# Performance work log

Hardware: AMD Instinct MI355X
Metric: run time of the kernel (lower is better)

## Reference

```python
import jax, jax.numpy as jnp
import numpy as np

WS = 8   # window_size
SS = 4   # shift_size
NH = 8   # num_heads


def _shift_mask(ws, ss):
    """Faithful port of _create_shift_mask (returns [1,1,ws,ws])."""
    m = np.zeros((ws, ws), np.float32)
    cnt = 0
    for hs in (slice(0, ws - ss), slice(ws - ss, ws)):
        for wsl in (slice(0, ws - ss), slice(ws - ss, ws)):
            m[hs, wsl] = cnt
            cnt += 1
    shifted = np.roll(m, (-ss, -ss), (0, 1))
    return (m != shifted).astype(np.float32)[None, None]

_MASK = jnp.asarray(_shift_mask(WS, SS))  # all-ones when ss == ws/2 (as in source)


def window_partition(x, ws):
    # [B,C,H,W] -> [B*nWin, C, ws, ws]
    B, C, H, W = x.shape
    x = x.reshape(B, C, H // ws, ws, W // ws, ws)
    x = x.transpose(0, 2, 4, 1, 3, 5)
    return x.reshape(-1, C, ws, ws)


def window_merge(x, H, W, ws):
    # [B*nWin, C, ws, ws] -> [B,C,H,W]
    C = x.shape[1]
    B = x.shape[0] // ((H // ws) * (W // ws))
    x = x.reshape(B, H // ws, W // ws, C, ws, ws)
    x = x.transpose(0, 3, 1, 4, 2, 5)
    return x.reshape(B, C, H, W)


def conv1x1(x, w):
    # 1x1 conv, no bias: weight [Cout, Cin]
    return jnp.einsum('oc,bchw->bohw', w, x)


def win_attention(q, k, v, temperature):
    # q,k,v: [Bw, C, ws, ws]; temperature: [nh,1,1]
    Bw, C, wh, ww = q.shape
    hd = C // NH
    N = wh * ww
    def heads(t):
        return t.reshape(Bw, NH, hd, N).transpose(0, 1, 3, 2)  # [Bw,nh,N,hd]
    q, k, v = heads(q), heads(k), heads(v)
    attn = jnp.einsum('bhnd,bhmd->bhnm', q, k) * temperature  # temp broadcasts per-head
    attn = jax.nn.softmax(attn, axis=-1)
    out = jnp.einsum('bhnm,bhmd->bhnd', attn, v)
    return out.transpose(0, 1, 3, 2).reshape(Bw, C, wh, ww)


def _branch(x_q, x_kv, temperature, Wq, Wk, Wv, Wo):
    xq_w = window_partition(x_q, WS)
    xkv_w = window_partition(x_kv, WS)
    q = conv1x1(xq_w, Wq)
    k = conv1x1(xkv_w, Wk)
    v = conv1x1(xkv_w, Wv)
    a = win_attention(q, k, v, temperature)
    return conv1x1(a, Wo)  # [B*nWin, C, ws, ws]


def setup_inputs() -> dict:
    key = jax.random.key(0)
    ks = jax.random.split(key, 6)
    B, C, H, W = 2, 256, 192, 192
    return {
        'x_q': jax.random.normal(ks[0], (B, C, H, W), jnp.float32),
        'x_kv': jax.random.normal(ks[1], (B, C, H, W), jnp.float32),
        'temperature': jnp.ones((NH, 1, 1), jnp.float32),
        'Wq': jax.random.normal(ks[2], (C, C), jnp.float32) * 0.02,
        'Wk': jax.random.normal(ks[3], (C, C), jnp.float32) * 0.02,
        'Wv': jax.random.normal(ks[4], (C, C), jnp.float32) * 0.02,
        'Wo': jax.random.normal(ks[5], (C, C), jnp.float32) * 0.02,
    }


def reference(x_q, x_kv, temperature, Wq, Wk, Wv, Wo):
    B, C, H, W = x_q.shape
    # unshifted branch
    out_win = _branch(x_q, x_kv, temperature, Wq, Wk, Wv, Wo)
    out = window_merge(out_win, H, W, WS)
    # shifted branch
    xq_s = jnp.roll(x_q, shift=(-SS, -SS), axis=(2, 3))
    xkv_s = jnp.roll(x_kv, shift=(-SS, -SS), axis=(2, 3))
    out_s = _branch(xq_s, xkv_s, temperature, Wq, Wk, Wv, Wo)
    out_s = out_s * (1.0 - _MASK)  # zero overlap regions (all-ones mask here)
    out_s = window_merge(out_s, H, W, WS)
    out_s = jnp.roll(out_s, shift=(SS, SS), axis=(2, 3))
    return out + out_s
```

## Files before the change

kernel.cpp:

```cpp
#include <hip/hip_runtime.h>
#include <hip/hip_bf16.h>


typedef short bf16x4 __attribute__((ext_vector_type(4)));
typedef short bf16x8 __attribute__((ext_vector_type(8)));
typedef float f32x4  __attribute__((ext_vector_type(4)));
typedef unsigned short ushort_t;

#define MFMA_K16(A_, B_, C_) __builtin_amdgcn_mfma_f32_16x16x16bf16_1k((A_), (B_), (C_), 0, 0, 0)
#define MFMA_K32(A_, B_, C_) __builtin_amdgcn_mfma_f32_16x16x32_bf16((A_), (B_), (C_), 0, 0, 0)

__device__ __forceinline__ short f2b(float f) {
  __hip_bfloat16 h = __float2bfloat16(f);
  return __builtin_bit_cast(short, h);
}
__device__ __forceinline__ bf16x4 cvt4(f32x4 v, float sc) {
  bf16x4 r;
  r[0] = f2b(v[0] * sc); r[1] = f2b(v[1] * sc);
  r[2] = f2b(v[2] * sc); r[3] = f2b(v[3] * sc);
  return r;
}
__device__ __forceinline__ int PI(int p) { return (p ^ (p >> 3)) & 7; }

template<bool B16>
__device__ __forceinline__ bf16x8 ldw8(const void* W, int row, int c0) {
  if constexpr (B16) {
    return *(const bf16x8*)((const ushort_t*)W + (row << 8) + c0);
  } else {
    const float* p = (const float*)W + (row << 8) + c0;
    const float4 x = *(const float4*)p, y = *(const float4*)(p + 4);
    bf16x8 f;
    f[0] = f2b(x.x); f[1] = f2b(x.y); f[2] = f2b(x.z); f[3] = f2b(x.w);
    f[4] = f2b(y.x); f[5] = f2b(y.y); f[6] = f2b(y.z); f[7] = f2b(y.w);
    return f;
  }
}
__device__ __forceinline__ bf16x8 ldw8b(const ushort_t* W, int row, int c0) {
  return *(const bf16x8*)(W + (row << 8) + c0);
}

constexpr size_t BUFE = 9437184;

__global__ void wconv(const float* __restrict__ a, const float* __restrict__ b,
                      const float* __restrict__ c, const float* __restrict__ d,
                      ushort_t* __restrict__ o) {
  const int gid = blockIdx.x * 256 + threadIdx.x;
  const int which = gid >> 14;
  const int idx = (gid & 16383) * 4;
  const float* src = which == 0 ? a : which == 1 ? b : which == 2 ? c : d;
  const float4 v = *(const float4*)(src + idx);
  bf16x4 w; w[0] = f2b(v.x); w[1] = f2b(v.y); w[2] = f2b(v.z); w[3] = f2b(v.w);
  *(bf16x4*)(o + which * 65536 + idx) = w;
}

__global__ __launch_bounds__(256, 4) void g0_xt(
    const float* __restrict__ xq, const float* __restrict__ xkv,
    ushort_t* __restrict__ xtq, ushort_t* __restrict__ xtkv, int bbase)
{
  __shared__ __align__(16) ushort_t tile[64 * 72];
  const int tid = threadIdx.x;
  const int id = (blockIdx.x & 7) * (gridDim.x >> 3) + (blockIdx.x >> 3);
  int r = id;
  const int pxt = r % 576; r /= 576;
  const int ct = r & 3; r >>= 2;
  const int which = r & 1;
  const int bl = r >> 1;
  const float* src = which ? xkv : xq;
  ushort_t* dst = which ? xtkv : xtq;
  const size_t gib = (size_t)(bbase + bl) * BUFE;

  {
    const int cr = tid >> 2, seg = tid & 3;
    const float* p = src + gib + (size_t)(ct * 64 + cr) * 36864 + pxt * 64 + seg * 16;
    const float4 f0 = *(const float4*)p,       f1 = *(const float4*)(p + 4);
    const float4 f2 = *(const float4*)(p + 8), f3 = *(const float4*)(p + 12);
    bf16x8 a, b;
    a[0]=f2b(f0.x); a[1]=f2b(f0.y); a[2]=f2b(f0.z); a[3]=f2b(f0.w);
    a[4]=f2b(f1.x); a[5]=f2b(f1.y); a[6]=f2b(f1.z); a[7]=f2b(f1.w);
    b[0]=f2b(f2.x); b[1]=f2b(f2.y); b[2]=f2b(f2.z); b[3]=f2b(f2.w);
    b[4]=f2b(f3.x); b[5]=f2b(f3.y); b[6]=f2b(f3.z); b[7]=f2b(f3.w);
    *(bf16x8*)(tile + cr * 72 + seg * 16) = a;
    *(bf16x8*)(tile + cr * 72 + seg * 16 + 8) = b;
  }
  __syncthreads();
  {
    const int opx = tid >> 2, oseg = tid & 3;
    bf16x8 a, b;
    #pragma unroll
    for (int j = 0; j < 8; ++j) a[j] = tile[(oseg * 16 + j) * 72 + opx];
    #pragma unroll
    for (int j = 0; j < 8; ++j) b[j] = tile[(oseg * 16 + 8 + j) * 72 + opx];
    ushort_t* q = dst + (size_t)bl * BUFE + (size_t)(pxt * 64 + opx) * 256 + ct * 64 + oseg * 16;
    *(bf16x8*)q = a;
    *(bf16x8*)(q + 8) = b;
  }
}

__global__ __launch_bounds__(256, 4) void g1_qkv(
    const ushort_t* __restrict__ xtq, const ushort_t* __restrict__ xtkv,
    const ushort_t* __restrict__ Wq, const ushort_t* __restrict__ Wk,
    const ushort_t* __restrict__ Wv,
    ushort_t* __restrict__ qbuf, ushort_t* __restrict__ kbuf,
    ushort_t* __restrict__ vimg)
{
  __shared__ __align__(16) char smem[26624];
  const int tid = threadIdx.x, lane = tid & 63, wv4 = tid >> 6;
  const int l15 = lane & 15, g = lane >> 4;

  const int wid = (blockIdx.x & 7) * (gridDim.x >> 3) + (blockIdx.x >> 3);
  const int ct = wid % 6;
  int r = wid / 6;
  const int whalf = r & 1; r >>= 1;
  const int h = r % 192;
  const int bl = r / 192;
  const int ph = h & 7;
  const int winbase = bl * 576 + (h >> 3) * 24 + whalf * 12;
  const int pxrow = h * 192 + whalf * 96;

  const int mode = ct >> 1;
  const ushort_t* xs = ((mode == 0) ? xtq : xtkv) + (size_t)bl * BUFE;
  const ushort_t* W  = (mode == 0) ? Wq : (mode == 1) ? Wk : Wv;
  const int chalf = (ct & 1) * 128;
  const int cobase = chalf + wv4 * 32;

  f32x4 acc[6][2];
  #pragma unroll
  for (int nt = 0; nt < 6; ++nt) { acc[nt][0] = {0,0,0,0}; acc[nt][1] = {0,0,0,0}; }

  #pragma unroll
  for (int ki = 0; ki < 2; ++ki) {
    bf16x8 wf[4][2];
    #pragma unroll
    for (int sk = 0; sk < 4; ++sk) {
      const int c0 = ki * 128 + sk * 32 + g * 8;
      wf[sk][0] = ldw8b(W, cobase + l15,      c0);
      wf[sk][1] = ldw8b(W, cobase + 16 + l15, c0);
    }
    if (ki) __syncthreads();
    #pragma unroll
    for (int j = 0; j < 6; ++j) {
      const int u = j * 256 + tid;
      const int t = u >> 4, ch = u & 15;
      const bf16x8 v = *(const bf16x8*)(xs + (size_t)(pxrow + t) * 256 + ki * 128 + ch * 8);
      const int sl = ch ^ (t & 7);
      *(bf16x8*)(smem + (unsigned)(t * 256 + sl * 16)) = v;
    }
    __syncthreads();
    #pragma unroll
    for (int sk = 0; sk < 4; ++sk) {
      #pragma unroll
      for (int nt = 0; nt < 6; ++nt) {
        const int t = nt * 16 + l15;
        const int lch = sk * 4 + g;
        const bf16x8 af = *(const bf16x8*)(smem + (unsigned)(t * 256 + ((lch ^ (t & 7)) << 4)));
        if (mode < 2) {
          acc[nt][0] = MFMA_K32(wf[sk][0], af, acc[nt][0]);
          acc[nt][1] = MFMA_K32(wf[sk][1], af, acc[nt][1]);
        } else {
          acc[nt][0] = MFMA_K32(af, wf[sk][0], acc[nt][0]);
          acc[nt][1] = MFMA_K32(af, wf[sk][1], acc[nt][1]);
        }
      }
    }
  }
  __syncthreads();

  if (mode < 2) {
    #pragma unroll
    for (int nt = 0; nt < 6; ++nt)
      #pragma unroll
      for (int cj = 0; cj < 2; ++cj) {
        const int t = nt * 16 + l15;
        const int bb = (wv4 * 4 + cj * 2 + (g >> 1)) ^ (t & 7);
        *(bf16x4*)(smem + (unsigned)(t * 256 + bb * 16 + (g & 1) * 8)) = cvt4(acc[nt][cj], 1.f);
      }
    __syncthreads();
    ushort_t* dst = (mode == 0) ? qbuf : kbuf;
    #pragma unroll
    for (int j = 0; j < 6; ++j) {
      const int u = j * 256 + tid;
      const int t = u >> 4, ch = u & 15;
      const bf16x8 v = *(const bf16x8*)(smem + (unsigned)(t * 256 + ((ch ^ (t & 7)) << 4)));
      const int win = winbase + (t >> 3);
      const int pos = ph * 8 + (t & 7);
      *(bf16x8*)(dst + (size_t)win * 16384 + pos * 256 + chalf + ch * 8) = v;
    }
  } else {
    #pragma unroll
    for (int nt = 0; nt < 6; ++nt)
      #pragma unroll
      for (int dj = 0; dj < 2; ++dj) {
        const int dl = wv4 * 32 + dj * 16 + l15;
        *(bf16x4*)(smem + (unsigned)(dl * 208 + (nt * 16 + 4 * g) * 2)) = cvt4(acc[nt][dj], 1.f);
      }
    __syncthreads();
    #pragma unroll
    for (int j = 0; j < 6; ++j) {
      const int u = j * 256 + tid;
      const int dl = u / 12, ch = u - dl * 12;
      const bf16x8 v = *(const bf16x8*)(smem + (unsigned)(dl * 208 + ch * 16));
      *(bf16x8*)(vimg + (size_t)bl * BUFE + (size_t)(chalf + dl) * 36864 + pxrow + ch * 8) = v;
    }
  }
}

__global__ __launch_bounds__(256, 4) void attn2(
    const float* __restrict__ temp,
    const ushort_t* __restrict__ qbuf, const ushort_t* __restrict__ kbuf,
    const ushort_t* __restrict__ vimg, ushort_t* __restrict__ abuf)
{
  const int tid = threadIdx.x, lane = tid & 63, wv4 = tid >> 6;
  const int l15 = lane & 15, g = lane >> 4;

  const int wid = (blockIdx.x & 7) * (gridDim.x >> 3) + (blockIdx.x >> 3);
  const int hg = wid & 1;
  const int winL = wid >> 1;
  const int bl = winL / 576, rw = winL % 576;
  const int wh = rw / 24, ww = rw % 24;
  const int h = hg * 4 + wv4;
  const float tm = temp[h];
  const size_t wb = (size_t)winL * 16384;
  const int hb = h * 32;
  const f32x4 fzero = {0.f, 0.f, 0.f, 0.f};

  bf16x8 qf[4], kf[4];
  #pragma unroll
  for (int i = 0; i < 4; ++i) {
    qf[i] = *(const bf16x8*)(qbuf + wb + (i * 16 + l15) * 256 + hb + g * 8);
    kf[i] = *(const bf16x8*)(kbuf + wb + (i * 16 + l15) * 256 + hb + g * 8);
  }
  f32x4 s[4][4];
  #pragma unroll
  for (int mt = 0; mt < 4; ++mt)
    #pragma unroll
    for (int nt = 0; nt < 4; ++nt)
      s[mt][nt] = MFMA_K32(kf[mt], qf[nt], fzero);

  bf16x4 Pb[4][4];
  #pragma unroll
  for (int nt = 0; nt < 4; ++nt) {
    float mx = -1e30f;
    #pragma unroll
    for (int mt = 0; mt < 4; ++mt)
      #pragma unroll
      for (int rr = 0; rr < 4; ++rr) {
        const float v = s[mt][nt][rr] * tm;
        s[mt][nt][rr] = v;
        mx = fmaxf(mx, v);
      }
    mx = fmaxf(mx, __shfl_xor(mx, 16));
    mx = fmaxf(mx, __shfl_xor(mx, 32));
    float sum = 0.f;
    #pragma unroll
    for (int mt = 0; mt < 4; ++mt)
      #pragma unroll
      for (int rr = 0; rr < 4; ++rr) {
        const float p = __expf(s[mt][nt][rr] - mx);
        s[mt][nt][rr] = p;
        sum += p;
      }
    sum += __shfl_xor(sum, 16);
    sum += __shfl_xor(sum, 32);
    const float ri = 1.f / sum;
    #pragma unroll
    for (int mt = 0; mt < 4; ++mt) Pb[mt][nt] = cvt4(s[mt][nt], ri);
  }

  f32x4 pcd[2][4];
  #pragma unroll
  for (int dj = 0; dj < 2; ++dj)
    #pragma unroll
    for (int nt = 0; nt < 4; ++nt) pcd[dj][nt] = fzero;
  #pragma unroll
  for (int mt = 0; mt < 4; ++mt)
    #pragma unroll
    for (int dj = 0; dj < 2; ++dj) {
      const int d = hb + dj * 16 + l15;
      const bf16x4 vf = *(const bf16x4*)(vimg + (size_t)bl * BUFE + (size_t)d * 36864
                        + (wh * 8 + 2 * mt + (g >> 1)) * 192 + ww * 8 + 4 * (g & 1));
      #pragma unroll
      for (int nt = 0; nt < 4; ++nt)
        pcd[dj][nt] = MFMA_K16(vf, Pb[mt][nt], pcd[dj][nt]);
    }

  #pragma unroll
  for (int dj = 0; dj < 2; ++dj)
    #pragma unroll
    for (int nt = 0; nt < 4; ++nt) {
      const int pos = nt * 16 + l15;
      const int c0 = hb + dj * 16 + 4 * g;
      *(bf16x4*)(abuf + wb + pos * 256 + c0) = cvt4(pcd[dj][nt], 1.f);
    }
}

__global__ __launch_bounds__(256, 4) void k2_out(
    const ushort_t* __restrict__ Wo, const ushort_t* __restrict__ abuf,
    float* __restrict__ out, int bbase)
{
  __shared__ __align__(16) char smem[24576];
  const int tid = threadIdx.x, lane = tid & 63, wv4 = tid >> 6;
  const int l15 = lane & 15, g = lane >> 4;

  const int wid = (blockIdx.x & 7) * (gridDim.x >> 3) + (blockIdx.x >> 3);
  const int ct = wid & 1;
  int r = wid >> 1;
  const int whalf = r & 1; r >>= 1;
  const int h = r % 192, bl = r / 192;
  const int wh = h >> 3, ph = h & 7, wstart = whalf * 96;
  const int winbase = bl * 576 + wh * 24 + (wstart >> 3);

  f32x4 acc[6][2];
  #pragma unroll
  for (int nt = 0; nt < 6; ++nt) { acc[nt][0] = {0,0,0,0}; acc[nt][1] = {0,0,0,0}; }

  const int corow0 = ct * 128 + wv4 * 32 + l15;

  #pragma unroll
  for (int ki = 0; ki < 2; ++ki) {
    const int kb = ki * 128;
    if (ki) __syncthreads();
    #pragma unroll
    for (int j = 0; j < 6; ++j) {
      const int u = j * 256 + tid;
      const int t = u >> 4, ch = u & 15;
      const int win = winbase + (t >> 3);
      const int wpos = ph * 8 + (t & 7);
      const bf16x8 v = *(const bf16x8*)(abuf + (size_t)win * 16384 + wpos * 256 + kb + ch * 8);
      const int sl = ch ^ (t & 7);
      *(bf16x8*)(smem + (unsigned)(t * 256 + sl * 16)) = v;
    }
    __syncthreads();
    #pragma unroll
    for (int sk = 0; sk < 4; ++sk) {
      const int c0 = kb + sk * 32 + g * 8;
      const bf16x8 w0 = ldw8b(Wo, corow0,      c0);
      const bf16x8 w1 = ldw8b(Wo, corow0 + 16, c0);
      #pragma unroll
      for (int nt = 0; nt < 6; ++nt) {
        const int t = nt * 16 + l15;
        const int lch = sk * 4 + g;
        const bf16x8 af = *(const bf16x8*)(smem + (unsigned)(t * 256 + ((lch ^ (t & 7)) << 4)));
        acc[nt][0] = MFMA_K32(w0, af, acc[nt][0]);
        acc[nt][1] = MFMA_K32(w1, af, acc[nt][1]);
      }
    }
  }

  #pragma unroll
  for (int nt = 0; nt < 6; ++nt)
    #pragma unroll
    for (int cj = 0; cj < 2; ++cj) {
      const int t = nt * 16 + l15;
      #pragma unroll
      for (int rr = 0; rr < 4; ++rr) {
        const int co = ct * 128 + wv4 * 32 + cj * 16 + 4 * g + rr;
        out[(size_t)(bbase + bl) * BUFE + (size_t)co * 36864 + h * 192 + wstart + t]
            = acc[nt][cj][rr];
      }
    }
}

constexpr int SMEM_OLD = 65536;

template<int NT>
__device__ __forceinline__ void stage_half(char* dst, const float* __restrict__ src,
                                           int coff, int tid, size_t ibase, int xoff) {
  #pragma unroll
  for (int j = 0; j < 1024 / NT; ++j) {
    const int u = j * NT + tid;
    const int c = u >> 3, hr = u & 7;
    const size_t gg = ibase + (size_t)(c + coff) * 36864 + (size_t)(xoff + hr * 192);
    const float4 a0 = *(const float4*)(src + gg);
    const float4 a1 = *(const float4*)(src + gg + 4);
    const float vv[8] = {a0.x, a0.y, a0.z, a0.w, a1.x, a1.y, a1.z, a1.w};
    #pragma unroll
    for (int w = 0; w < 8; ++w) {
      const int pos = hr * 8 + w;
      const unsigned ad = (unsigned)(pos * 256 + (((c >> 3) ^ PI(pos)) << 4) + (c & 7) * 2);
      *(short*)(dst + ad) = f2b(vv[w]);
    }
  }
}
__device__ __forceinline__ bf16x8 xfrag8(const char* base, int kt, int nt, int l15, int g) {
  const int pos = nt * 16 + l15;
  const int c0 = kt * 32 + g * 8;
  const unsigned ad = (unsigned)(pos * 256 + (((c0 >> 3) ^ PI(pos)) << 4));
  return *(const bf16x8*)(base + ad);
}

template<bool WB16>
__global__ __launch_bounds__(512, 4) void wsmdta_old(
    const float* __restrict__ xq, const float* __restrict__ xkv,
    const float* __restrict__ temp,
    const void* __restrict__ Wq, const void* __restrict__ Wk,
    const void* __restrict__ Wv, const void* __restrict__ Wo,
    float* __restrict__ out)
{
  extern __shared__ __align__(16) char smem[];
  const int tid = threadIdx.x, lane = tid & 63, wv = tid >> 6;
  const int l15 = lane & 15, g = lane >> 4;
  const int bid = blockIdx.x;
  const int wid = (bid & 7) * 144 + (bid >> 3);
  const int b  = wid / 576, rw = wid - b * 576;
  const int wh = rw / 24,   ww = rw - wh * 24;
  const int xoff = wh * 1536 + ww * 8;
  const size_t ibase = (size_t)b * BUFE;
  const unsigned VB = 32768u + (unsigned)wv * 4096u;
  const f32x4 fzero = {0.f, 0.f, 0.f, 0.f};
  const int h = wv;
  const float tm = temp[h];

  f32x4 qcd[2][4];
  #pragma unroll
  for (int dj = 0; dj < 2; ++dj)
    #pragma unroll
    for (int nt = 0; nt < 4; ++nt) qcd[dj][nt] = fzero;
  #pragma unroll
  for (int half = 0; half < 2; ++half) {
    if (half) __syncthreads();
    stage_half<512>(smem, xq, half * 128, tid, ibase, xoff);
    __syncthreads();
    const int cg = half * 128;
    #pragma unroll
    for (int kt = 0; kt < 4; ++kt) {
      const bf16x8 w0 = ldw8<WB16>(Wq, h * 32 + l15,      cg + kt * 32 + g * 8);
      const bf16x8 w1 = ldw8<WB16>(Wq, h * 32 + 16 + l15, cg + kt * 32 + g * 8);
      #pragma unroll
      for (int nt = 0; nt < 4; ++nt) {
        const bf16x8 xf = xfrag8(smem, kt, nt, l15, g);
        qcd[0][nt] = MFMA_K32(w0, xf, qcd[0][nt]);
        qcd[1][nt] = MFMA_K32(w1, xf, qcd[1][nt]);
      }
    }
    __syncthreads();
  }
  bf16x4 qb[2][4];
  #pragma unroll
  for (int dj = 0; dj < 2; ++dj)
    #pragma unroll
    for (int nt = 0; nt < 4; ++nt) qb[dj][nt] = cvt4(qcd[dj][nt], 1.f);

  f32x4 kcd[2][4], vcd[2][4];
  #pragma unroll
  for (int dj = 0; dj < 2; ++dj)
    #pragma unroll
    for (int nt = 0; nt < 4; ++nt) { kcd[dj][nt] = fzero; vcd[dj][nt] = fzero; }
  #pragma unroll
  for (int half = 0; half < 2; ++half) {
    stage_half<512>(smem, xkv, half * 128, tid, ibase, xoff);
    __syncthreads();
    const int cg = half * 128;
    #pragma unroll
    for (int kt = 0; kt < 4; ++kt) {
      const bf16x8 wk0 = ldw8<WB16>(Wk, h * 32 + l15,      cg + kt * 32 + g * 8);
      const bf16x8 wk1 = ldw8<WB16>(Wk, h * 32 + 16 + l15, cg + kt * 32 + g * 8);
      const bf16x8 wv0 = ldw8<WB16>(Wv, h * 32 + l15,      cg + kt * 32 + g * 8);
      const bf16x8 wv1 = ldw8<WB16>(Wv, h * 32 + 16 + l15, cg + kt * 32 + g * 8);
      #pragma unroll
      for (int np = 0; np < 2; ++np) {
        const bf16x8 xf0 = xfrag8(smem, kt, np * 2,     l15, g);
        const bf16x8 xf1 = xfrag8(smem, kt, np * 2 + 1, l15, g);
        kcd[0][np*2]   = MFMA_K32(wk0, xf0, kcd[0][np*2]);
        kcd[1][np*2]   = MFMA_K32(wk1, xf0, kcd[1][np*2]);
        vcd[0][np*2]   = MFMA_K32(wv0, xf0, vcd[0][np*2]);
        vcd[1][np*2]   = MFMA_K32(wv1, xf0, vcd[1][np*2]);
        kcd[0][np*2+1] = MFMA_K32(wk0, xf1, kcd[0][np*2+1]);
        kcd[1][np*2+1] = MFMA_K32(wk1, xf1, kcd[1][np*2+1]);
        vcd[0][np*2+1] = MFMA_K32(wv0, xf1, vcd[0][np*2+1]);
        vcd[1][np*2+1] = MFMA_K32(wv1, xf1, vcd[1][np*2+1]);
      }
    }
    if (half == 0) __syncthreads();
  }
  bf16x4 kb[2][4];
  #pragma unroll
  for (int dj = 0; dj < 2; ++dj)
    #pragma unroll
    for (int mt = 0; mt < 4; ++mt) kb[dj][mt] = cvt4(kcd[dj][mt], 1.f);
  #pragma unroll
  for (int dj = 0; dj < 2; ++dj)
    #pragma unroll
    for (int mt = 0; mt < 4; ++mt) {
      const bf16x4 q = cvt4(vcd[dj][mt], 1.f);
      const int m = mt * 16 + l15;
      #pragma unroll
      for (int rr = 0; rr < 4; ++rr) {
        const int d = dj * 16 + 4 * g + rr;
        const unsigned ad = VB + (unsigned)(d * 128 + (((m >> 3) ^ (d & 7)) << 4) + (m & 7) * 2);
        *(short*)(smem + ad) = q[rr];
      }
    }
  f32x4 s[4][4];
  #pragma unroll
  for (int mt = 0; mt < 4; ++mt)
    #pragma unroll
    for (int nt = 0; nt < 4; ++nt) {
      s[mt][nt] = MFMA_K16(kb[0][mt], qb[0][nt], fzero);
      s[mt][nt] = MFMA_K16(kb[1][mt], qb[1][nt], s[mt][nt]);
    }
  bf16x4 Pb[4][4];
  #pragma unroll
  for (int nt = 0; nt < 4; ++nt) {
    float mx = -1e30f;
    #pragma unroll
    for (int mt = 0; mt < 4; ++mt)
      #pragma unroll
      for (int rr = 0; rr < 4; ++rr) {
        const float v = s[mt][nt][rr] * tm;
        s[mt][nt][rr] = v;
        mx = fmaxf(mx, v);
      }
    mx = fmaxf(mx, __shfl_xor(mx, 16));
    mx = fmaxf(mx, __shfl_xor(mx, 32));
    float sum = 0.f;
    #pragma unroll
    for (int mt = 0; mt < 4; ++mt)
      #pragma unroll
      for (int rr = 0; rr < 4; ++rr) {
        const float p = __expf(s[mt][nt][rr] - mx);
        s[mt][nt][rr] = p;
        sum += p;
      }
    sum += __shfl_xor(sum, 16);
    sum += __shfl_xor(sum, 32);
    const float ri = 1.f / sum;
    #pragma unroll
    for (int mt = 0; mt < 4; ++mt) Pb[mt][nt] = cvt4(s[mt][nt], ri);
  }
  f32x4 pcd[2][4];
  #pragma unroll
  for (int dj = 0; dj < 2; ++dj)
    #pragma unroll
    for (int nt = 0; nt < 4; ++nt) pcd[dj][nt] = fzero;
  #pragma unroll
  for (int mt = 0; mt < 4; ++mt)
    #pragma unroll
    for (int dj = 0; dj < 2; ++dj) {
      const int d = dj * 16 + l15;
      const unsigned ad = VB + (unsigned)(d * 128 + (((mt * 2 + (g >> 1)) ^ (d & 7)) << 4) + (g & 1) * 8);
      const bf16x4 vf = *(const bf16x4*)(smem + ad);
      #pragma unroll
      for (int nt = 0; nt < 4; ++nt)
        pcd[dj][nt] = MFMA_K16(vf, Pb[mt][nt], pcd[dj][nt]);
    }
  __syncthreads();
  #pragma unroll
  for (int dj = 0; dj < 2; ++dj)
    #pragma unroll
    for (int nt = 0; nt < 4; ++nt) {
      const bf16x4 q = cvt4(pcd[dj][nt], 1.f);
      const int pos = nt * 16 + l15;
      const int c0 = h * 32 + dj * 16 + 4 * g;
      const unsigned ad = (unsigned)(pos * 512 + (((c0 >> 3) ^ PI(pos)) << 4) + (c0 & 7) * 2);
      *(bf16x4*)(smem + ad) = q;
    }
  __syncthreads();
  f32x4 ocd[4][2];
  #pragma unroll
  for (int nt = 0; nt < 4; ++nt) { ocd[nt][0] = fzero; ocd[nt][1] = fzero; }
  {
    bf16x8 w0 = ldw8<WB16>(Wo, wv * 32 + l15,      g * 8);
    bf16x8 w1 = ldw8<WB16>(Wo, wv * 32 + 16 + l15, g * 8);
    #pragma unroll
    for (int ks = 0; ks < 8; ++ks) {
      bf16x8 n0, n1;
      if (ks < 7) {
        n0 = ldw8<WB16>(Wo, wv * 32 + l15,      (ks + 1) * 32 + g * 8);
        n1 = ldw8<WB16>(Wo, wv * 32 + 16 + l15, (ks + 1) * 32 + g * 8);
      }
      #pragma unroll
      for (int nt = 0; nt < 4; ++nt) {
        const int pos = nt * 16 + l15;
        const unsigned ad = (unsigned)(pos * 512 + (((ks * 4 + g) ^ PI(pos)) << 4));
        const bf16x8 af = *(const bf16x8*)(smem + ad);
        ocd[nt][0] = MFMA_K32(af, w0, ocd[nt][0]);
        ocd[nt][1] = MFMA_K32(af, w1, ocd[nt][1]);
      }
      if (ks < 7) { w0 = n0; w1 = n1; }
    }
  }
  #pragma unroll
  for (int nt = 0; nt < 4; ++nt)
    #pragma unroll
    for (int ctj = 0; ctj < 2; ++ctj) {
      const int c_out = wv * 32 + ctj * 16 + l15;
      const int h_out = nt * 2 + (g >> 1);
      const int w0o = 4 * (g & 1);
      float4 v;
      v.x = ocd[nt][ctj][0]; v.y = ocd[nt][ctj][1];
      v.z = ocd[nt][ctj][2]; v.w = ocd[nt][ctj][3];
      *(float4*)(out + ibase + (size_t)c_out * 36864 + (size_t)(xoff + h_out * 192 + w0o)) = v;
    }
}

extern "C" void kernel_launch(void* const* d_in, const int* in_sizes, int n_in,
                              void* d_out, int out_size, void* d_ws, size_t ws_size,
                              hipStream_t stream) {
  (void)in_sizes; (void)n_in; (void)out_size;
  const float* xq   = (const float*)d_in[0];
  const float* xkv  = (const float*)d_in[1];
  const float* temp = (const float*)d_in[2];
  const float* Wq   = (const float*)d_in[3];
  const float* Wk   = (const float*)d_in[4];
  const float* Wv   = (const float*)d_in[5];
  const float* Wo   = (const float*)d_in[6];
  float* out = (float*)d_out;

  const size_t W_ELEMS = 262144;
  auto need = [&](int nb) {
    return (W_ELEMS + 5u * (size_t)nb * BUFE) * sizeof(ushort_t);
  };
  ushort_t* wsb = (ushort_t*)d_ws;

  auto run = [&](int bbase, int nb) {
    ushort_t* base = wsb + W_ELEMS;
    ushort_t* xtq  = base;
    ushort_t* xtkv = xtq  + (size_t)nb * BUFE;
    ushort_t* qb   = xtkv + (size_t)nb * BUFE;
    ushort_t* kb   = qb   + (size_t)nb * BUFE;
    ushort_t* vb   = kb   + (size_t)nb * BUFE;
    g0_xt<<<dim3(nb * 4608), dim3(256), 0, stream>>>(xq, xkv, xtq, xtkv, bbase);
    g1_qkv<<<dim3(nb * 2304), dim3(256), 0, stream>>>(
        xtq, xtkv, wsb, wsb + 65536, wsb + 131072, qb, kb, vb);
    attn2<<<dim3(nb * 1152), dim3(256), 0, stream>>>(temp, qb, kb, vb, qb);
    k2_out<<<dim3(nb * 768), dim3(256), 0, stream>>>(wsb + 196608, qb, out, bbase);
  };

  if (ws_size >= need(2)) {
    wconv<<<dim3(256), dim3(256), 0, stream>>>(Wq, Wk, Wv, Wo, wsb);
    run(0, 2);
  } else if (ws_size >= need(1)) {
    wconv<<<dim3(256), dim3(256), 0, stream>>>(Wq, Wk, Wv, Wo, wsb);
    run(0, 1);
    run(1, 1);
  } else if (ws_size >= W_ELEMS * sizeof(ushort_t)) {
    wconv<<<dim3(256), dim3(256), 0, stream>>>(Wq, Wk, Wv, Wo, wsb);
    (void)hipFuncSetAttribute((const void*)&wsmdta_old<true>,
                              hipFuncAttributeMaxDynamicSharedMemorySize, SMEM_OLD);
    wsmdta_old<true><<<dim3(1152), dim3(512), SMEM_OLD, stream>>>(
        xq, xkv, temp, wsb, wsb + 65536, wsb + 131072, wsb + 196608, out);
  } else {
    (void)hipFuncSetAttribute((const void*)&wsmdta_old<false>,
                              hipFuncAttributeMaxDynamicSharedMemorySize, SMEM_OLD);
    wsmdta_old<false><<<dim3(1152), dim3(512), SMEM_OLD, stream>>>(
        xq, xkv, temp, Wq, Wk, Wv, Wo, out);
  }
}
```

Measured before the change: 184.5 us.

## Fuse input transpose and bf16 conversion into QKV projection kernel

Removes the separate g0_xt pass that converted fp32 NCHW inputs into bf16 pixel-major buffers, and makes g1_qkv read the fp32 inputs directly. It converts them to bf16 and scatters them into swizzled shared memory with a new XOR swizzle. This drops one kernel launch plus a full write and re-read of two bf16 intermediate images, and cuts the workspace requirement. In exchange, each QKV block now reads fp32 (twice the bytes), and the reads are repeated across the six channel tiles. The shared-memory writes become scalar 2-byte stores, which may cause bank conflicts.

```diff
diff --git a/kernel.cpp b/kernel.cpp
--- a/kernel.cpp
+++ b/kernel.cpp
@@ -53,55 +53,12 @@
   *(bf16x4*)(o + which * 65536 + idx) = w;
 }
 
-__global__ __launch_bounds__(256, 4) void g0_xt(
+__global__ __launch_bounds__(256, 4) void g1_qkv(
     const float* __restrict__ xq, const float* __restrict__ xkv,
-    ushort_t* __restrict__ xtq, ushort_t* __restrict__ xtkv, int bbase)
-{
-  __shared__ __align__(16) ushort_t tile[64 * 72];
-  const int tid = threadIdx.x;
-  const int id = (blockIdx.x & 7) * (gridDim.x >> 3) + (blockIdx.x >> 3);
-  int r = id;
-  const int pxt = r % 576; r /= 576;
-  const int ct = r & 3; r >>= 2;
-  const int which = r & 1;
-  const int bl = r >> 1;
-  const float* src = which ? xkv : xq;
-  ushort_t* dst = which ? xtkv : xtq;
-  const size_t gib = (size_t)(bbase + bl) * BUFE;
-
-  {
-    const int cr = tid >> 2, seg = tid & 3;
-    const float* p = src + gib + (size_t)(ct * 64 + cr) * 36864 + pxt * 64 + seg * 16;
-    const float4 f0 = *(const float4*)p,       f1 = *(const float4*)(p + 4);
-    const float4 f2 = *(const float4*)(p + 8), f3 = *(const float4*)(p + 12);
-    bf16x8 a, b;
-    a[0]=f2b(f0.x); a[1]=f2b(f0.y); a[2]=f2b(f0.z); a[3]=f2b(f0.w);
-    a[4]=f2b(f1.x); a[5]=f2b(f1.y); a[6]=f2b(f1.z); a[7]=f2b(f1.w);
-    b[0]=f2b(f2.x); b[1]=f2b(f2.y); b[2]=f2b(f2.z); b[3]=f2b(f2.w);
-    b[4]=f2b(f3.x); b[5]=f2b(f3.y); b[6]=f2b(f3.z); b[7]=f2b(f3.w);
-    *(bf16x8*)(tile + cr * 72 + seg * 16) = a;
-    *(bf16x8*)(tile + cr * 72 + seg * 16 + 8) = b;
-  }
-  __syncthreads();
-  {
-    const int opx = tid >> 2, oseg = tid & 3;
-    bf16x8 a, b;
-    #pragma unroll
-    for (int j = 0; j < 8; ++j) a[j] = tile[(oseg * 16 + j) * 72 + opx];
-    #pragma unroll
-    for (int j = 0; j < 8; ++j) b[j] = tile[(oseg * 16 + 8 + j) * 72 + opx];
-    ushort_t* q = dst + (size_t)bl * BUFE + (size_t)(pxt * 64 + opx) * 256 + ct * 64 + oseg * 16;
-    *(bf16x8*)q = a;
-    *(bf16x8*)(q + 8) = b;
-  }
-}
-
-__global__ __launch_bounds__(256, 4) void g1_qkv(
-    const ushort_t* __restrict__ xtq, const ushort_t* __restrict__ xtkv,
     const ushort_t* __restrict__ Wq, const ushort_t* __restrict__ Wk,
     const ushort_t* __restrict__ Wv,
     ushort_t* __restrict__ qbuf, ushort_t* __restrict__ kbuf,
-    ushort_t* __restrict__ vimg)
+    ushort_t* __restrict__ vimg, int bbase)
 {
   __shared__ __align__(16) char smem[26624];
   const int tid = threadIdx.x, lane = tid & 63, wv4 = tid >> 6;
@@ -118,8 +75,8 @@
   const int pxrow = h * 192 + whalf * 96;
 
   const int mode = ct >> 1;
-  const ushort_t* xs = ((mode == 0) ? xtq : xtkv) + (size_t)bl * BUFE;
-  const ushort_t* W  = (mode == 0) ? Wq : (mode == 1) ? Wk : Wv;
+  const float* xsrc = ((mode == 0) ? xq : xkv) + (size_t)(bbase + bl) * BUFE;
+  const ushort_t* W = (mode == 0) ? Wq : (mode == 1) ? Wk : Wv;
   const int chalf = (ct & 1) * 128;
   const int cobase = chalf + wv4 * 32;
 
@@ -140,10 +97,18 @@
     #pragma unroll
     for (int j = 0; j < 6; ++j) {
       const int u = j * 256 + tid;
-      const int t = u >> 4, ch = u & 15;
-      const bf16x8 v = *(const bf16x8*)(xs + (size_t)(pxrow + t) * 256 + ki * 128 + ch * 8);
-      const int sl = ch ^ (t & 7);
-      *(bf16x8*)(smem + (unsigned)(t * 256 + sl * 16)) = v;
+      const int c = u / 12, tch = u - 12 * c;
+      const float* p = xsrc + (size_t)(ki * 128 + c) * 36864 + pxrow + tch * 8;
+      const float4 a0 = *(const float4*)p;
+      const float4 a1 = *(const float4*)(p + 4);
+      const float vv[8] = {a0.x, a0.y, a0.z, a0.w, a1.x, a1.y, a1.z, a1.w};
+      const int cb = c >> 3, cl = (c & 7) * 2;
+      #pragma unroll
+      for (int w = 0; w < 8; ++w) {
+        const int t = tch * 8 + w;
+        const int p2 = (t ^ (t >> 3)) & 7;
+        *(short*)(smem + (unsigned)(t * 256 + ((cb ^ p2) << 4) + cl)) = f2b(vv[w]);
+      }
     }
     __syncthreads();
     #pragma unroll
@@ -151,8 +116,9 @@
       #pragma unroll
       for (int nt = 0; nt < 6; ++nt) {
         const int t = nt * 16 + l15;
+        const int p2 = (t ^ (t >> 3)) & 7;
         const int lch = sk * 4 + g;
-        const bf16x8 af = *(const bf16x8*)(smem + (unsigned)(t * 256 + ((lch ^ (t & 7)) << 4)));
+        const bf16x8 af = *(const bf16x8*)(smem + (unsigned)(t * 256 + ((lch ^ p2) << 4)));
         if (mode < 2) {
           acc[nt][0] = MFMA_K32(wf[sk][0], af, acc[nt][0]);
           acc[nt][1] = MFMA_K32(wf[sk][1], af, acc[nt][1]);
@@ -608,20 +574,16 @@
 
   const size_t W_ELEMS = 262144;
   auto need = [&](int nb) {
-    return (W_ELEMS + 5u * (size_t)nb * BUFE) * sizeof(ushort_t);
+    return (W_ELEMS + 3u * (size_t)nb * BUFE) * sizeof(ushort_t);
   };
   ushort_t* wsb = (ushort_t*)d_ws;
 
   auto run = [&](int bbase, int nb) {
-    ushort_t* base = wsb + W_ELEMS;
-    ushort_t* xtq  = base;
-    ushort_t* xtkv = xtq  + (size_t)nb * BUFE;
-    ushort_t* qb   = xtkv + (size_t)nb * BUFE;
-    ushort_t* kb   = qb   + (size_t)nb * BUFE;
-    ushort_t* vb   = kb   + (size_t)nb * BUFE;
-    g0_xt<<<dim3(nb * 4608), dim3(256), 0, stream>>>(xq, xkv, xtq, xtkv, bbase);
+    ushort_t* qb = wsb + W_ELEMS;
+    ushort_t* kb = qb + (size_t)nb * BUFE;
+    ushort_t* vb = kb + (size_t)nb * BUFE;
     g1_qkv<<<dim3(nb * 2304), dim3(256), 0, stream>>>(
-        xtq, xtkv, wsb, wsb + 65536, wsb + 131072, qb, kb, vb);
+        xq, xkv, wsb, wsb + 65536, wsb + 131072, qb, kb, vb, bbase);
     attn2<<<dim3(nb * 1152), dim3(256), 0, stream>>>(temp, qb, kb, vb, qb);
     k2_out<<<dim3(nb * 768), dim3(256), 0, stream>>>(wsb + 196608, qb, out, bbase);
   };
```

Measured after the change: 354.4 us. 92.1% more time.
